# Performance work log

Measured on AMD Instinct MI355X. Metric: run time of the kernel, lower is better.

## Reference

```python
import jax, jax.numpy as jnp
import numpy as np

B, T, SD, DD = 256, 365, 64, 16
H, NH, L, FF = 256, 8, 4, 1024
K, P, N = 5, 30, 10000
DEG = np.pi / 180.0


def _ln(x, g, b):
    mu = x.mean(-1, keepdims=True)
    var = ((x - mu) ** 2).mean(-1, keepdims=True)
    return g * (x - mu) / jnp.sqrt(var + 1e-5) + b


def _gelu(x):
    return jax.nn.gelu(x, approximate=False)


def _forward(static, dynamic, lat, lon, all_statics, station_coords,
             W_st, b_st, g_st, be_st, W_dy, b_dy, g_dy, be_dy,
             Wqkv, bqkv, Wo, bo, g_ln1, be_ln1, Wf1, bf1, Wf2, bf2, g_ln2, be_ln2,
             W_o1, b_o1, W_o2, b_o2, scale, shift):
    # denormalize to CONUS degrees, then radians (as BallTree haversine expects)
    lat_o = (lat + 1.0) / 2.0 * (49.0 - 24.0) + 24.0
    lon_o = (lon + 1.0) / 2.0 * (-66.5 + 125.0) - 125.0
    qlat = lat_o[:, 0] * DEG
    qlon = lon_o[:, 0] * DEG
    slat = station_coords[:, 0]
    slon = station_coords[:, 1]
    dlat = qlat[:, None] - slat[None, :]
    dlon = qlon[:, None] - slon[None, :]
    # haversine term; true distance = 2*asin(sqrt(hav)) is monotone in hav,
    # so ranking by hav reproduces BallTree(metric='haversine') neighbor order
    hav = jnp.sin(dlat / 2) ** 2 + jnp.cos(qlat)[:, None] * jnp.cos(slat)[None, :] * jnp.sin(dlon / 2) ** 2
    _, nbr = jax.lax.top_k(-hav, K + 1)          # [B, K+1] nearest stations
    nbr = nbr[:, 1:]                              # drop self (nearest), keep K
    neigh = all_statics[nbr].reshape(static.shape[0], K * SD)  # gather + flatten
    combined = jnp.concatenate([static, neigh], axis=-1)       # [B, (K+1)*SD]

    sfeat = _gelu(_ln(combined @ W_st + b_st, g_st, be_st))    # static_net (dropout=eval)
    x = _gelu(_ln(dynamic @ W_dy + b_dy, g_dy, be_dy)) + sfeat[:, None, :]

    hd = H // NH
    inv_sqrt_d = 1.0 / jnp.sqrt(jnp.float32(hd))
    Bq, Tq = x.shape[0], x.shape[1]
    for l in range(L):  # post-norm TransformerEncoderLayer, relu FF
        qkv = x @ Wqkv[l] + bqkv[l]
        q, k, v = jnp.split(qkv, 3, axis=-1)
        q = q.reshape(Bq, Tq, NH, hd)
        k = k.reshape(Bq, Tq, NH, hd)
        v = v.reshape(Bq, Tq, NH, hd)
        att = jax.nn.softmax(jnp.einsum('bqhd,bkhd->bhqk', q, k) * inv_sqrt_d, axis=-1)
        ao = jnp.einsum('bhqk,bkhd->bqhd', att, v).reshape(Bq, Tq, H) @ Wo[l] + bo[l]
        x = _ln(x + ao, g_ln1[l], be_ln1[l])
        ff = jax.nn.relu(x @ Wf1[l] + bf1[l]) @ Wf2[l] + bf2[l]
        x = _ln(x + ff, g_ln2[l], be_ln2[l])

    pooled = x.mean(axis=1)
    raw = jnp.tanh(_gelu((pooled + sfeat) @ W_o1 + b_o1) @ W_o2 + b_o2)
    return raw * scale + shift


def setup_inputs() -> dict:
    key = jax.random.key(0)
    ks = jax.random.split(key, 24)
    rn = lambda k, shp: jax.random.normal(k, shp, jnp.float32) * 0.02
    inp = {}
    inp['static'] = jax.random.normal(ks[0], (B, SD), jnp.float32)
    inp['dynamic'] = jax.random.normal(ks[1], (B, T, DD), jnp.float32)
    inp['lat'] = jax.random.uniform(ks[2], (B, 1), jnp.float32, -1.0, 1.0)
    inp['lon'] = jax.random.uniform(ks[3], (B, 1), jnp.float32, -1.0, 1.0)
    inp['all_statics'] = jax.random.normal(ks[4], (N, SD), jnp.float32)
    slat = jax.random.uniform(ks[5], (N,), jnp.float32, 24.0, 49.0) * DEG
    slon = jax.random.uniform(ks[6], (N,), jnp.float32, -125.0, -66.5) * DEG
    inp['station_coords'] = jnp.stack([slat, slon], axis=-1)
    # static_net
    inp['W_st'] = rn(ks[7], (SD * (K + 1), H)); inp['b_st'] = jnp.zeros(H)
    inp['g_st'] = jnp.ones(H); inp['be_st'] = jnp.zeros(H)
    # dynamic_emb
    inp['W_dy'] = rn(ks[8], (DD, H)); inp['b_dy'] = jnp.zeros(H)
    inp['g_dy'] = jnp.ones(H); inp['be_dy'] = jnp.zeros(H)
    # transformer (stacked over layers)
    inp['Wqkv'] = rn(ks[9], (L, H, 3 * H)); inp['bqkv'] = jnp.zeros((L, 3 * H))
    inp['Wo'] = rn(ks[10], (L, H, H)); inp['bo'] = jnp.zeros((L, H))
    inp['g_ln1'] = jnp.ones((L, H)); inp['be_ln1'] = jnp.zeros((L, H))
    inp['Wf1'] = rn(ks[11], (L, H, FF)); inp['bf1'] = jnp.zeros((L, FF))
    inp['Wf2'] = rn(ks[12], (L, FF, H)); inp['bf2'] = jnp.zeros((L, H))
    inp['g_ln2'] = jnp.ones((L, H)); inp['be_ln2'] = jnp.zeros((L, H))
    # output head
    inp['W_o1'] = rn(ks[13], (H, H // 2)); inp['b_o1'] = jnp.zeros(H // 2)
    inp['W_o2'] = rn(ks[14], (H // 2, P)); inp['b_o2'] = jnp.zeros(P)
    inp['scale'] = jnp.array(1.0, jnp.float32)
    inp['shift'] = jnp.array(0.0, jnp.float32)
    return inp


def reference(static, dynamic, lat, lon, all_statics, station_coords,
              W_st, b_st, g_st, be_st, W_dy, b_dy, g_dy, be_dy,
              Wqkv, bqkv, Wo, bo, g_ln1, be_ln1, Wf1, bf1, Wf2, bf2, g_ln2, be_ln2,
              W_o1, b_o1, W_o2, b_o2, scale, shift):
    return _forward(static, dynamic, lat, lon, all_statics, station_coords,
                    W_st, b_st, g_st, be_st, W_dy, b_dy, g_dy, be_dy,
                    Wqkv, bqkv, Wo, bo, g_ln1, be_ln1, Wf1, bf1, Wf2, bf2, g_ln2, be_ln2,
                    W_o1, b_o1, W_o2, b_o2, scale, shift)
```

## Files before the change

kernel.cpp:

```cpp
#include <hip/hip_runtime.h>
#include <math.h>

#define T_SEQ 365
#define HDIM 256
#define NHEADS 8
#define HD 32
#define BATCH 256
#define DDIM 16
#define FFDIM 1024
#define NST 10000
#define KNB 5
#define SDIM 64

typedef __bf16 bf16x8 __attribute__((ext_vector_type(8)));
typedef float  f32x16 __attribute__((ext_vector_type(16)));
typedef unsigned short u16x8 __attribute__((ext_vector_type(8)));

__device__ __forceinline__ ushort f2b_hi(float v) {
    unsigned u = __float_as_uint(v);
    unsigned r = u + 0x7fffu + ((u >> 16) & 1u);
    return (ushort)(r >> 16);
}
__device__ __forceinline__ float b2f(ushort h) {
    return __uint_as_float(((unsigned)h) << 16);
}
__device__ __forceinline__ ushort f2b_lo(float v, ushort hi) {
    return f2b_hi(v - b2f(hi));
}

__device__ __forceinline__ float gelu_f(float x) {
    return 0.5f * x * (1.f + erff(x * 0.70710678118654752f));
}


__device__ __forceinline__ float block_sum256(float v, float* sred) {
    #pragma unroll
    for (int off = 32; off; off >>= 1) v += __shfl_xor(v, off);
    int wave = threadIdx.x >> 6;
    if ((threadIdx.x & 63) == 0) sred[wave] = v;
    __syncthreads();
    float s = sred[0] + sred[1] + sred[2] + sred[3];
    __syncthreads();
    return s;
}

__global__ __launch_bounds__(256) void topk_kernel(
    const float* __restrict__ lat, const float* __restrict__ lon,
    const float* __restrict__ coords, int* __restrict__ nbr)
{
    __shared__ float hav[NST];
    __shared__ float rv[256];
    __shared__ int   ri[256];
    const float DEG = 0.017453292519943295f;
    int b = blockIdx.x, t = threadIdx.x;
    float lat_o = (lat[b] + 1.f) * 0.5f * 25.f + 24.f;
    float lon_o = (lon[b] + 1.f) * 0.5f * 58.5f - 125.f;
    float qlat = lat_o * DEG, qlon = lon_o * DEG;
    float cq = cosf(qlat);
    for (int i = t; i < NST; i += 256) {
        float slat = coords[2*i], slon = coords[2*i+1];
        float dlat = qlat - slat, dlon = qlon - slon;
        float s1 = sinf(dlat * 0.5f), s2 = sinf(dlon * 0.5f);
        hav[i] = s1*s1 + cq * cosf(slat) * s2*s2;
    }
    __syncthreads();
    for (int sel = 0; sel < KNB + 1; ++sel) {
        float bv = 1e30f; int bi = 0x7fffffff;
        for (int i = t; i < NST; i += 256) {
            float v = hav[i];
            if (v < bv || (v == bv && i < bi)) { bv = v; bi = i; }
        }
        rv[t] = bv; ri[t] = bi;
        __syncthreads();
        for (int s = 128; s > 0; s >>= 1) {
            if (t < s) {
                float ov = rv[t+s]; int oi = ri[t+s];
                if (ov < rv[t] || (ov == rv[t] && oi < ri[t])) { rv[t] = ov; ri[t] = oi; }
            }
            __syncthreads();
        }
        if (t == 0) {
            if (sel > 0) nbr[b*KNB + sel - 1] = ri[0];
            hav[ri[0]] = 1e30f;
        }
        __syncthreads();
    }
}

__global__ __launch_bounds__(256) void sfeat_kernel(
    const float* __restrict__ stat, const float* __restrict__ all_st,
    const int* __restrict__ nbr, const float* __restrict__ W,
    const float* __restrict__ bias, const float* __restrict__ g,
    const float* __restrict__ be, float* __restrict__ sfeat)
{
    __shared__ float comb[(KNB+1)*SDIM];
    __shared__ float sred[4];
    int b = blockIdx.x, t = threadIdx.x;
    for (int i = t; i < (KNB+1)*SDIM; i += 256) {
        if (i < SDIM) comb[i] = stat[b*SDIM + i];
        else {
            int n = (i - SDIM) >> 6, d = (i - SDIM) & 63;
            comb[i] = all_st[(size_t)nbr[b*KNB + n] * SDIM + d];
        }
    }
    __syncthreads();
    float acc = bias[t];
    for (int j = 0; j < (KNB+1)*SDIM; ++j)
        acc = fmaf(comb[j], W[j*HDIM + t], acc);
    float mu  = block_sum256(acc, sred) * (1.f/256.f);
    float d   = acc - mu;
    float var = block_sum256(d*d, sred) * (1.f/256.f);
    float y = g[t] * d * rsqrtf(var + 1e-5f) + be[t];
    sfeat[(size_t)b*HDIM + t] = gelu_f(y);
}

__global__ __launch_bounds__(256) void dyn_kernel(
    const float* __restrict__ dynv, const float* __restrict__ W,
    const float* __restrict__ bias, const float* __restrict__ g,
    const float* __restrict__ be, const float* __restrict__ sfeat,
    ushort* __restrict__ xhi, ushort* __restrict__ xlo)
{
    __shared__ float w[DDIM*HDIM];
    __shared__ float dr[4][DDIM];
    int wave = threadIdx.x >> 6, lane = threadIdx.x & 63;
    int row0 = blockIdx.x * 4;
    for (int i = threadIdx.x; i < DDIM*HDIM; i += 256) w[i] = W[i];
    if (lane < DDIM)
        dr[wave][lane] = dynv[(size_t)(row0 + wave)*DDIM + lane];
    __syncthreads();
    int row = row0 + wave;
    int b = row / T_SEQ;
    int c0 = lane * 4;
    float v0 = bias[c0], v1 = bias[c0+1], v2 = bias[c0+2], v3 = bias[c0+3];
    #pragma unroll
    for (int k = 0; k < DDIM; ++k) {
        float dk = dr[wave][k];
        float4 wv = *reinterpret_cast<const float4*>(&w[k*HDIM + c0]);
        v0 = fmaf(dk, wv.x, v0); v1 = fmaf(dk, wv.y, v1);
        v2 = fmaf(dk, wv.z, v2); v3 = fmaf(dk, wv.w, v3);
    }
    float s = v0 + v1 + v2 + v3;
    #pragma unroll
    for (int off = 32; off; off >>= 1) s += __shfl_xor(s, off);
    float mu = s * (1.f/256.f);
    float d0 = v0-mu, d1 = v1-mu, d2 = v2-mu, d3 = v3-mu;
    float s2 = d0*d0 + d1*d1 + d2*d2 + d3*d3;
    #pragma unroll
    for (int off = 32; off; off >>= 1) s2 += __shfl_xor(s2, off);
    float rs = rsqrtf(s2 * (1.f/256.f) + 1e-5f);
    float4 gg = *reinterpret_cast<const float4*>(&g[c0]);
    float4 bb = *reinterpret_cast<const float4*>(&be[c0]);
    float4 sf = *reinterpret_cast<const float4*>(&sfeat[(size_t)b*HDIM + c0]);
    float o0 = gelu_f(gg.x*d0*rs + bb.x) + sf.x;
    float o1 = gelu_f(gg.y*d1*rs + bb.y) + sf.y;
    float o2 = gelu_f(gg.z*d2*rs + bb.z) + sf.z;
    float o3 = gelu_f(gg.w*d3*rs + bb.w) + sf.w;
    size_t o = ((size_t)(row >> 5) * 32 + (c0 >> 3)) * 256 + ((row & 31) << 3) + (c0 & 7);
    ushort4 hv, lv;
    hv.x = f2b_hi(o0); lv.x = f2b_lo(o0, hv.x);
    hv.y = f2b_hi(o1); lv.y = f2b_lo(o1, hv.y);
    hv.z = f2b_hi(o2); lv.z = f2b_lo(o2, hv.z);
    hv.w = f2b_hi(o3); lv.w = f2b_lo(o3, hv.w);
    *reinterpret_cast<ushort4*>(&xhi[o]) = hv;
    *reinterpret_cast<ushort4*>(&xlo[o]) = lv;
}

__global__ __launch_bounds__(256) void tsplit_kernel(
    const float* __restrict__ W, ushort* __restrict__ hi, ushort* __restrict__ lo,
    int K, int N)
{
    __shared__ float tile[32][33];
    size_t l = blockIdx.z;
    const float* Wl = W + l*(size_t)K*N;
    ushort* hil = hi + l*(size_t)K*N;
    ushort* lol = lo + l*(size_t)K*N;
    int n0 = blockIdx.x*32, k0 = blockIdx.y*32;
    int tx = threadIdx.x & 31, ty = threadIdx.x >> 5;
    int KB = K >> 3;
    for (int i = ty; i < 32; i += 8) tile[i][tx] = Wl[(size_t)(k0+i)*N + n0 + tx];
    __syncthreads();
    for (int i = ty; i < 32; i += 8) {
        float v = tile[tx][i];
        ushort h = f2b_hi(v);
        size_t o = ((size_t)(n0 >> 5) * KB + (k0 >> 3) + (tx >> 3)) * 256
                 + ((size_t)i << 3) + (tx & 7);
        hil[o] = h;
        lol[o] = f2b_lo(v, h);
    }
}

template<int DO_RELU, int OUT>
__global__ __launch_bounds__(256) void gemm_mfma(
    const ushort* __restrict__ Ahi, const ushort* __restrict__ Alo,
    const ushort* __restrict__ Bhi, const ushort* __restrict__ Blo,
    const float* __restrict__ bias,
    ushort* __restrict__ Chi, ushort* __restrict__ Clo,
    ushort* __restrict__ Wq_h, ushort* __restrict__ Wq_l,
    ushort* __restrict__ Wk_h, ushort* __restrict__ Wk_l,
    ushort* __restrict__ Wv_h, ushort* __restrict__ Wv_l,
    int M, int N, int K)
{
    const int t = threadIdx.x;
    const int lane = t & 63, wave = t >> 6;
    const int wr = wave >> 1, wc = wave & 1;
    const int lr = lane & 31, kg = lane >> 5;
    const int row_b = blockIdx.y * 128 + wr * 64;
    const int col_b = blockIdx.x * 128 + wc * 64;
    const int KB = K >> 3;

    const ushort *pAh[2], *pAl[2], *pBh[2], *pBl[2];
    #pragma unroll
    for (int mi = 0; mi < 2; ++mi) {
        int rb = row_b + mi*32; if (rb > M - 32) rb = M - 32;
        size_t base = ((size_t)(rb >> 5) * KB + kg) * 256 + lr * 8;
        pAh[mi] = Ahi + base; pAl[mi] = Alo + base;
    }
    #pragma unroll
    for (int nj = 0; nj < 2; ++nj) {
        size_t base = ((size_t)((col_b + nj*32) >> 5) * KB + kg) * 256 + lr * 8;
        pBh[nj] = Bhi + base; pBl[nj] = Blo + base;
    }

    f32x16 acc[2][2];
    #pragma unroll
    for (int i = 0; i < 2; ++i)
        #pragma unroll
        for (int j = 0; j < 2; ++j)
            #pragma unroll
            for (int r = 0; r < 16; ++r) acc[i][j][r] = 0.f;

    bf16x8 a0h[2], a0l[2], b0h[2], b0l[2];
    bf16x8 a1h[2], a1l[2], b1h[2], b1l[2];

#define LOADF(AH, AL, BH, BL, OFF) do {                                        \
    _Pragma("unroll") for (int mi = 0; mi < 2; ++mi) {                         \
        AH[mi] = *reinterpret_cast<const bf16x8*>(pAh[mi] + (OFF));            \
        AL[mi] = *reinterpret_cast<const bf16x8*>(pAl[mi] + (OFF)); }          \
    _Pragma("unroll") for (int nj = 0; nj < 2; ++nj) {                         \
        BH[nj] = *reinterpret_cast<const bf16x8*>(pBh[nj] + (OFF));            \
        BL[nj] = *reinterpret_cast<const bf16x8*>(pBl[nj] + (OFF)); } } while(0)

#define MFMAF(AH, AL, BH, BL) do {                                             \
    _Pragma("unroll") for (int mi = 0; mi < 2; ++mi)                           \
    _Pragma("unroll") for (int nj = 0; nj < 2; ++nj) {                         \
        acc[mi][nj] = __builtin_amdgcn_mfma_f32_32x32x16_bf16(                 \
            AH[mi], BH[nj], acc[mi][nj], 0, 0, 0);                             \
        acc[mi][nj] = __builtin_amdgcn_mfma_f32_32x32x16_bf16(                 \
            AH[mi], BL[nj], acc[mi][nj], 0, 0, 0);                             \
        acc[mi][nj] = __builtin_amdgcn_mfma_f32_32x32x16_bf16(                 \
            AL[mi], BH[nj], acc[mi][nj], 0, 0, 0); } } while(0)

    LOADF(a0h, a0l, b0h, b0l, 0);
    for (int k0 = 0; k0 < K; k0 += 32) {
        size_t o1 = (size_t)((k0 + 16) >> 3) * 256;
        LOADF(a1h, a1l, b1h, b1l, o1);
        MFMAF(a0h, a0l, b0h, b0l);
        size_t o2 = (k0 + 32 < K) ? (size_t)((k0 + 32) >> 3) * 256 : 0;
        LOADF(a0h, a0l, b0h, b0l, o2);
        MFMAF(a1h, a1l, b1h, b1l);
    }
#undef LOADF
#undef MFMAF

    #pragma unroll
    for (int mi = 0; mi < 2; ++mi) {
        int rb2 = row_b + mi*32;
        #pragma unroll
        for (int nj = 0; nj < 2; ++nj) {
            int colf = col_b + nj*32 + lr;
            float bv = bias[colf];
            if (OUT == 1) {
                size_t ftb = ((size_t)(rb2 >> 5) * (N >> 3) + (colf >> 3)) * 256 + (colf & 7);
                #pragma unroll
                for (int r = 0; r < 16; ++r) {
                    int r31 = (r & 3) + 8*(r >> 2) + 4*kg;
                    int row = rb2 + r31;
                    if (row >= M) continue;
                    float v = acc[mi][nj][r] + bv;
                    if (DO_RELU) v = fmaxf(v, 0.f);
                    size_t oo = ftb + (size_t)r31 * 8;
                    ushort hh = f2b_hi(v);
                    Chi[oo] = hh;
                    Clo[oo] = f2b_lo(v, hh);
                }
            } else {
                int sel = (col_b + nj*32) >> 8;
                int h = (colf >> 5) & 7;
                int d = colf & 31;
                #pragma unroll
                for (int r = 0; r < 16; ++r) {
                    int r31 = (r & 3) + 8*(r >> 2) + 4*kg;
                    int row = rb2 + r31;
                    if (row >= M) continue;
                    float v = acc[mi][nj][r] + bv;
                    int bl = row / T_SEQ;
                    int tok = row - bl * T_SEQ;
                    size_t bb = (size_t)(bl*8 + h) * 12288;
                    ushort hh = f2b_hi(v);
                    ushort ll = f2b_lo(v, hh);
                    if (sel == 0) {
                        size_t o = bb + (size_t)((tok >> 5)*4 + (d >> 3))*256
                                 + ((tok & 31) << 3) + (d & 7);
                        Wq_h[o] = hh; Wq_l[o] = ll;
                    } else if (sel == 1) {
                        size_t o = bb + (size_t)((tok >> 5)*4 + (d >> 3))*256
                                 + ((tok & 31) << 3) + (d & 7);
                        Wk_h[o] = hh; Wk_l[o] = ll;
                    } else {
                        size_t o = bb + (size_t)(tok >> 3)*256 + d*8 + (tok & 7);
                        Wv_h[o] = hh; Wv_l[o] = ll;
                    }
                }
            }
        }
    }
}

__global__ __launch_bounds__(256) void gemm_ln(
    const ushort* __restrict__ Ahi, const ushort* __restrict__ Alo,
    const ushort* __restrict__ Bhi, const ushort* __restrict__ Blo,
    const float* __restrict__ bias,
    ushort* __restrict__ xhi, ushort* __restrict__ xlo,
    const float* __restrict__ g, const float* __restrict__ be,
    int M, int K)
{
    const int N = HDIM;
    const int t = threadIdx.x;
    const int lane = t & 63, wave = t >> 6;
    const int lr = lane & 31, kg = lane >> 5;
    const int row_b = blockIdx.y * 32;
    const int col_w = wave * 64;
    const int KB = K >> 3;

    const ushort *pAh, *pAl, *pBh[2], *pBl[2];
    {
        size_t base = ((size_t)(row_b >> 5) * KB + kg) * 256 + lr * 8;
        pAh = Ahi + base; pAl = Alo + base;
    }
    #pragma unroll
    for (int nj = 0; nj < 2; ++nj) {
        size_t base = ((size_t)((col_w + nj*32) >> 5) * KB + kg) * 256 + lr * 8;
        pBh[nj] = Bhi + base; pBl[nj] = Blo + base;
    }

    f32x16 acc[2];
    #pragma unroll
    for (int j = 0; j < 2; ++j)
        #pragma unroll
        for (int r = 0; r < 16; ++r) acc[j][r] = 0.f;

    bf16x8 a0h, a0l, b0h[2], b0l[2];
    bf16x8 a1h, a1l, b1h[2], b1l[2];

#define LOADF(AH, AL, BH, BL, OFF) do {                                        \
    AH = *reinterpret_cast<const bf16x8*>(pAh + (OFF));                        \
    AL = *reinterpret_cast<const bf16x8*>(pAl + (OFF));                        \
    _Pragma("unroll") for (int nj = 0; nj < 2; ++nj) {                         \
        BH[nj] = *reinterpret_cast<const bf16x8*>(pBh[nj] + (OFF));            \
        BL[nj] = *reinterpret_cast<const bf16x8*>(pBl[nj] + (OFF)); } } while(0)

#define MFMAF(AH, AL, BH, BL) do {                                             \
    _Pragma("unroll") for (int nj = 0; nj < 2; ++nj) {                         \
        acc[nj] = __builtin_amdgcn_mfma_f32_32x32x16_bf16(                     \
            AH, BH[nj], acc[nj], 0, 0, 0);                                     \
        acc[nj] = __builtin_amdgcn_mfma_f32_32x32x16_bf16(                     \
            AH, BL[nj], acc[nj], 0, 0, 0);                                     \
        acc[nj] = __builtin_amdgcn_mfma_f32_32x32x16_bf16(                     \
            AL, BH[nj], acc[nj], 0, 0, 0); } } while(0)

    LOADF(a0h, a0l, b0h, b0l, 0);
    for (int k0 = 0; k0 < K; k0 += 32) {
        size_t o1 = (size_t)((k0 + 16) >> 3) * 256;
        LOADF(a1h, a1l, b1h, b1l, o1);
        MFMAF(a0h, a0l, b0h, b0l);
        size_t o2 = (k0 + 32 < K) ? (size_t)((k0 + 32) >> 3) * 256 : 0;
        LOADF(a0h, a0l, b0h, b0l, o2);
        MFMAF(a1h, a1l, b1h, b1l);
    }
#undef LOADF
#undef MFMAF

    float s1[16], s2[16];
    #pragma unroll
    for (int nj = 0; nj < 2; ++nj) {
        int col = col_w + nj*32 + lr;
        float bv = bias[col];
        #pragma unroll
        for (int r = 0; r < 16; ++r) {
            int r31 = (r & 3) + 8*(r >> 2) + 4*kg;
            int row = row_b + r31;
            size_t oo = ((size_t)(row >> 5) * (N >> 3) + (col >> 3)) * 256
                      + ((row & 31) << 3) + (col & 7);
            float v = acc[nj][r] + bv + b2f(xhi[oo]) + b2f(xlo[oo]);
            acc[nj][r] = v;
            if (nj == 0) { s1[r] = v;  s2[r] = v*v; }
            else         { s1[r] += v; s2[r] += v*v; }
        }
    }
    #pragma unroll
    for (int r = 0; r < 16; ++r) {
        #pragma unroll
        for (int off = 1; off <= 16; off <<= 1) {
            s1[r] += __shfl_xor(s1[r], off);
            s2[r] += __shfl_xor(s2[r], off);
        }
    }
    __shared__ float red1[4][32];
    __shared__ float red2[4][32];
    __shared__ float tot1[32];
    __shared__ float tot2[32];
    if (lr == 0) {
        #pragma unroll
        for (int r = 0; r < 16; ++r) {
            int rr = (r & 3) + 8*(r >> 2) + 4*kg;
            red1[wave][rr] = s1[r];
            red2[wave][rr] = s2[r];
        }
    }
    __syncthreads();
    if (t < 32) {
        tot1[t] = red1[0][t] + red1[1][t] + red1[2][t] + red1[3][t];
        tot2[t] = red2[0][t] + red2[1][t] + red2[2][t] + red2[3][t];
    }
    __syncthreads();
    #pragma unroll
    for (int r = 0; r < 16; ++r) {
        int r31 = (r & 3) + 8*(r >> 2) + 4*kg;
        int row = row_b + r31;
        float mu = tot1[r31] * (1.f/256.f);
        float var = fmaf(-mu, mu, tot2[r31] * (1.f/256.f));
        float rs = rsqrtf(var + 1e-5f);
        #pragma unroll
        for (int nj = 0; nj < 2; ++nj) {
            int col = col_w + nj*32 + lr;
            float o = g[col] * (acc[nj][r] - mu) * rs + be[col];
            size_t oo = ((size_t)(row >> 5) * (N >> 3) + (col >> 3)) * 256
                      + ((row & 31) << 3) + (col & 7);
            ushort hh = f2b_hi(o);
            xhi[oo] = hh;
            xlo[oo] = f2b_lo(o, hh);
        }
    }
}

__global__ __launch_bounds__(256) void attn_mfma(
    const ushort* __restrict__ Qh, const ushort* __restrict__ Ql,
    const ushort* __restrict__ Kh, const ushort* __restrict__ Kl,
    const ushort* __restrict__ Vh, const ushort* __restrict__ Vl,
    ushort* __restrict__ ahi, ushort* __restrict__ alo)
{
    const int bh = blockIdx.y;
    const int wave = threadIdx.x >> 6, lane = threadIdx.x & 63;
    const int qt = blockIdx.x * 4 + wave;
    const int lr = lane & 31, kg = lane >> 5;
    const size_t base = (size_t)bh * 12288;
    const float scale = 0.17677669529663687f;

    bf16x8 qfh[2], qfl[2];
    #pragma unroll
    for (int ks = 0; ks < 2; ++ks) {
        size_t o = base + (size_t)(qt*4 + ks*2 + kg)*256 + lr*8;
        qfh[ks] = *reinterpret_cast<const bf16x8*>(Qh + o);
        qfl[ks] = *reinterpret_cast<const bf16x8*>(Ql + o);
    }

    float m = -3e38f;
    for (int kt = 0; kt < 12; ++kt) {
        f32x16 st;
        #pragma unroll
        for (int r = 0; r < 16; ++r) st[r] = 0.f;
        #pragma unroll
        for (int ks = 0; ks < 2; ++ks) {
            size_t o = base + (size_t)(kt*4 + ks*2 + kg)*256 + lr*8;
            bf16x8 kfh = *reinterpret_cast<const bf16x8*>(Kh + o);
            bf16x8 kfl = *reinterpret_cast<const bf16x8*>(Kl + o);
            st = __builtin_amdgcn_mfma_f32_32x32x16_bf16(kfh, qfh[ks], st, 0,0,0);
            st = __builtin_amdgcn_mfma_f32_32x32x16_bf16(kfh, qfl[ks], st, 0,0,0);
            st = __builtin_amdgcn_mfma_f32_32x32x16_bf16(kfl, qfh[ks], st, 0,0,0);
        }
        #pragma unroll
        for (int r = 0; r < 16; ++r) {
            int krow = kt*32 + (r & 3) + 8*(r >> 2) + 4*kg;
            m = fmaxf(m, (krow < T_SEQ) ? st[r] : -3e38f);
        }
    }
    m = fmaxf(m, __shfl_xor(m, 32));

    f32x16 oacc;
    #pragma unroll
    for (int r = 0; r < 16; ++r) oacc[r] = 0.f;
    float l = 0.f;

    for (int kt = 0; kt < 12; ++kt) {
        f32x16 st;
        #pragma unroll
        for (int r = 0; r < 16; ++r) st[r] = 0.f;
        #pragma unroll
        for (int ks = 0; ks < 2; ++ks) {
            size_t o = base + (size_t)(kt*4 + ks*2 + kg)*256 + lr*8;
            bf16x8 kfh = *reinterpret_cast<const bf16x8*>(Kh + o);
            bf16x8 kfl = *reinterpret_cast<const bf16x8*>(Kl + o);
            st = __builtin_amdgcn_mfma_f32_32x32x16_bf16(kfh, qfh[ks], st, 0,0,0);
            st = __builtin_amdgcn_mfma_f32_32x32x16_bf16(kfh, qfl[ks], st, 0,0,0);
            st = __builtin_amdgcn_mfma_f32_32x32x16_bf16(kfl, qfh[ks], st, 0,0,0);
        }
        float p[16];
        #pragma unroll
        for (int r = 0; r < 16; ++r) {
            int krow = kt*32 + (r & 3) + 8*(r >> 2) + 4*kg;
            float sv = (krow < T_SEQ) ? st[r] : -3e38f;
            float e = __expf((sv - m) * scale);
            p[r] = e; l += e;
        }
        float pp[16];
        #pragma unroll
        for (int r = 0; r < 16; ++r) pp[r] = __shfl_xor(p[r], 32);
        #pragma unroll
        for (int ks = 0; ks < 2; ++ks) {
            union { u16x8 u; bf16x8 b; } fh, fl;
            #pragma unroll
            for (int j = 0; j < 8; ++j) {
                float e;
                if (ks == 0)
                    e = kg ? ((j < 4) ? pp[4+j] : p[j])
                           : ((j < 4) ? p[j]    : pp[j-4]);
                else
                    e = kg ? ((j < 4) ? pp[12+j] : p[8+j])
                           : ((j < 4) ? p[8+j]   : pp[4+j]);
                ushort hh = f2b_hi(e);
                fh.u[j] = hh;
                fl.u[j] = f2b_lo(e, hh);
            }
            size_t vo = base + (size_t)(kt*4 + ks*2 + kg)*256 + lr*8;
            bf16x8 vfh = *reinterpret_cast<const bf16x8*>(Vh + vo);
            bf16x8 vfl = *reinterpret_cast<const bf16x8*>(Vl + vo);
            oacc = __builtin_amdgcn_mfma_f32_32x32x16_bf16(fh.b, vfh, oacc, 0,0,0);
            oacc = __builtin_amdgcn_mfma_f32_32x32x16_bf16(fh.b, vfl, oacc, 0,0,0);
            oacc = __builtin_amdgcn_mfma_f32_32x32x16_bf16(fl.b, vfh, oacc, 0,0,0);
        }
    }
    l += __shfl_xor(l, 32);
    float il = 1.f / l;

    const int bl = bh >> 3, h = bh & 7;
    #pragma unroll
    for (int r = 0; r < 16; ++r) {
        int q = (r & 3) + 8*(r >> 2) + 4*kg;
        float sc = __shfl(il, q);
        int row_local = qt*32 + q;
        if (row_local < T_SEQ) {
            float v = oacc[r] * sc;
            int grow = bl*T_SEQ + row_local;
            int col = h*32 + lr;
            size_t o = ((size_t)(grow >> 5)*32 + (col >> 3))*256
                     + ((grow & 31) << 3) + (col & 7);
            ushort hh = f2b_hi(v);
            ahi[o] = hh;
            alo[o] = f2b_lo(v, hh);
        }
    }
}

__global__ __launch_bounds__(256) void head_kernel(
    const ushort* __restrict__ xhi, const ushort* __restrict__ xlo,
    const float* __restrict__ sfeat,
    const float* __restrict__ W1, const float* __restrict__ b1,
    const float* __restrict__ W2, const float* __restrict__ b2,
    const float* __restrict__ scale, const float* __restrict__ shift,
    float* __restrict__ out)
{
    __shared__ float p[HDIM];
    __shared__ float h1[HDIM/2];
    int b = blockIdx.x, t = threadIdx.x;
    float acc = 0.f;
    for (int tt = 0; tt < T_SEQ; ++tt) {
        size_t row = (size_t)b*T_SEQ + tt;
        size_t o = ((row >> 5) * 32 + (t >> 3)) * 256 + ((row & 31) << 3) + (t & 7);
        acc += b2f(xhi[o]) + b2f(xlo[o]);
    }
    p[t] = acc * (1.f/365.f) + sfeat[(size_t)b*HDIM + t];
    __syncthreads();
    if (t < HDIM/2) {
        float a = b1[t];
        for (int c = 0; c < HDIM; ++c) a = fmaf(p[c], W1[c*(HDIM/2) + t], a);
        h1[t] = gelu_f(a);
    }
    __syncthreads();
    if (t < 30) {
        float a = b2[t];
        for (int j = 0; j < HDIM/2; ++j) a = fmaf(h1[j], W2[j*30 + t], a);
        out[b*30 + t] = tanhf(a) * scale[0] + shift[0];
    }
}

extern "C" void kernel_launch(void* const* d_in, const int* in_sizes, int n_in,
                              void* d_out, int out_size, void* d_ws, size_t ws_size,
                              hipStream_t stream) {
    const float* p_static = (const float*)d_in[0];
    const float* p_dyn    = (const float*)d_in[1];
    const float* p_lat    = (const float*)d_in[2];
    const float* p_lon    = (const float*)d_in[3];
    const float* p_all    = (const float*)d_in[4];
    const float* p_coords = (const float*)d_in[5];
    const float* p_Wst    = (const float*)d_in[6];
    const float* p_bst    = (const float*)d_in[7];
    const float* p_gst    = (const float*)d_in[8];
    const float* p_best   = (const float*)d_in[9];
    const float* p_Wdy    = (const float*)d_in[10];
    const float* p_bdy    = (const float*)d_in[11];
    const float* p_gdy    = (const float*)d_in[12];
    const float* p_bedy   = (const float*)d_in[13];
    const float* p_Wqkv   = (const float*)d_in[14];
    const float* p_bqkv   = (const float*)d_in[15];
    const float* p_Wo     = (const float*)d_in[16];
    const float* p_bo     = (const float*)d_in[17];
    const float* p_gln1   = (const float*)d_in[18];
    const float* p_beln1  = (const float*)d_in[19];
    const float* p_Wf1    = (const float*)d_in[20];
    const float* p_bf1    = (const float*)d_in[21];
    const float* p_Wf2    = (const float*)d_in[22];
    const float* p_bf2    = (const float*)d_in[23];
    const float* p_gln2   = (const float*)d_in[24];
    const float* p_beln2  = (const float*)d_in[25];
    const float* p_Wo1    = (const float*)d_in[26];
    const float* p_bo1    = (const float*)d_in[27];
    const float* p_Wo2    = (const float*)d_in[28];
    const float* p_bo2    = (const float*)d_in[29];
    const float* p_scale  = (const float*)d_in[30];
    const float* p_shift  = (const float*)d_in[31];
    float* out = (float*)d_out;
    (void)in_sizes; (void)n_in; (void)out_size;

    char* ws = (char*)d_ws;
    size_t off = 0;
    auto alloc = [&](size_t bytes) -> void* {
        void* p = ws + off;
        off += (bytes + 255) & ~(size_t)255;
        return p;
    };
    const int ROWS = BATCH * T_SEQ;
    int*    nbr   = (int*)   alloc((size_t)BATCH*KNB*sizeof(int));
    float*  sfeat = (float*) alloc((size_t)BATCH*HDIM*sizeof(float));
    ushort* xhi   = (ushort*)alloc((size_t)ROWS*HDIM*sizeof(ushort));
    ushort* xlo   = (ushort*)alloc((size_t)ROWS*HDIM*sizeof(ushort));
    const size_t SZ_QKV = (size_t)4*768*256, SZ_O = (size_t)4*256*256;
    const size_t SZ_F1  = (size_t)4*1024*256, SZ_F2 = (size_t)4*256*1024;
    ushort* Wqkvt_h = (ushort*)alloc(SZ_QKV*2*sizeof(ushort)); ushort* Wqkvt_l = Wqkvt_h + SZ_QKV;
    ushort* Wot_h   = (ushort*)alloc(SZ_O  *2*sizeof(ushort)); ushort* Wot_l   = Wot_h   + SZ_O;
    ushort* Wf1t_h  = (ushort*)alloc(SZ_F1 *2*sizeof(ushort)); ushort* Wf1t_l  = Wf1t_h  + SZ_F1;
    ushort* Wf2t_h  = (ushort*)alloc(SZ_F2 *2*sizeof(ushort)); ushort* Wf2t_l  = Wf2t_h  + SZ_F2;
    size_t fixed = off;

    const size_t PER_B = (size_t)T_SEQ * 1024 * 4;
    const size_t PER_A = (size_t)T_SEQ * 256 * 4;
    const size_t PER_CH = PER_B + PER_A;
    int CH = 32;
    {
        const int tiers[5] = {256, 192, 128, 96, 64};
        for (int i = 0; i < 5; ++i) {
            if (fixed + (size_t)tiers[i]*PER_CH + 8192 <= ws_size) { CH = tiers[i]; break; }
        }
    }
    char*   big    = (char*)alloc((size_t)CH * PER_B);
    ushort* aatt_h = (ushort*)alloc((size_t)CH * PER_A);
    const int RW = CH * T_SEQ;
    ushort* aatt_l = aatt_h + (size_t)RW * HDIM;
    const size_t seg = (size_t)CH * 8 * 12288;
    ushort* Qh  = (ushort*)big;
    ushort* Ql  = Qh  + seg;
    ushort* Kh2 = Ql  + seg;
    ushort* Kl2 = Kh2 + seg;
    ushort* Vth = Kl2 + seg;
    ushort* Vtl = Vth + seg;
    ushort* hbuf_h = (ushort*)big;
    ushort* hbuf_l = hbuf_h + (size_t)RW * FFDIM;
    const int GY  = (RW + 127) / 128;
    const int GY3 = RW / 32;

    topk_kernel <<<BATCH, 256, 0, stream>>>(p_lat, p_lon, p_coords, nbr);
    sfeat_kernel<<<BATCH, 256, 0, stream>>>(p_static, p_all, nbr, p_Wst, p_bst, p_gst, p_best, sfeat);
    dyn_kernel  <<<ROWS/4, 256, 0, stream>>>(p_dyn, p_Wdy, p_bdy, p_gdy, p_bedy, sfeat, xhi, xlo);
    tsplit_kernel<<<dim3(24, 8, 4), 256, 0, stream>>>(p_Wqkv, Wqkvt_h, Wqkvt_l, 256, 768);
    tsplit_kernel<<<dim3( 8, 8, 4), 256, 0, stream>>>(p_Wo,   Wot_h,   Wot_l,   256, 256);
    tsplit_kernel<<<dim3(32, 8, 4), 256, 0, stream>>>(p_Wf1,  Wf1t_h,  Wf1t_l,  256, 1024);
    tsplit_kernel<<<dim3( 8,32, 4), 256, 0, stream>>>(p_Wf2,  Wf2t_h,  Wf2t_l,  1024, 256);

    const int NCHUNK = BATCH / CH;
    for (int c = 0; c < NCHUNK; ++c) {
        size_t co = (size_t)c * CH * T_SEQ * HDIM;
        ushort* xhic = xhi + co;
        ushort* xloc = xlo + co;
        for (int l = 0; l < 4; ++l) {
            gemm_mfma<0,2><<<dim3(6, GY), 256, 0, stream>>>(
                xhic, xloc, Wqkvt_h + (size_t)l*768*256, Wqkvt_l + (size_t)l*768*256,
                p_bqkv + l*768, nullptr, nullptr,
                Qh, Ql, Kh2, Kl2, Vth, Vtl, RW, 768, 256);
            attn_mfma<<<dim3(3, CH*8), 256, 0, stream>>>(
                Qh, Ql, Kh2, Kl2, Vth, Vtl, aatt_h, aatt_l);
            gemm_ln<<<dim3(1, GY3), 256, 0, stream>>>(
                aatt_h, aatt_l, Wot_h + (size_t)l*256*256, Wot_l + (size_t)l*256*256,
                p_bo + l*256, xhic, xloc, p_gln1 + l*256, p_beln1 + l*256, RW, 256);
            gemm_mfma<1,1><<<dim3(8, GY), 256, 0, stream>>>(
                xhic, xloc, Wf1t_h + (size_t)l*1024*256, Wf1t_l + (size_t)l*1024*256,
                p_bf1 + l*1024, hbuf_h, hbuf_l,
                nullptr, nullptr, nullptr, nullptr, nullptr, nullptr, RW, 1024, 256);
            gemm_ln<<<dim3(1, GY3), 256, 0, stream>>>(
                hbuf_h, hbuf_l, Wf2t_h + (size_t)l*256*1024, Wf2t_l + (size_t)l*256*1024,
                p_bf2 + l*256, xhic, xloc, p_gln2 + l*256, p_beln2 + l*256, RW, 1024);
        }
    }
    head_kernel<<<BATCH, 256, 0, stream>>>(xhi, xlo, sfeat, p_Wo1, p_bo1, p_Wo2, p_bo2, p_scale, p_shift, out);
}
```

Baseline: 4.988 ms.

## Use single-pass online softmax in attention and chunk the activation buffer

The attention kernel now computes scores once per key tile with a running max and rescaling, replacing a separate pass that recomputed QK^T just to find the max. The residual stream buffer is allocated per chunk, with the embedding and mean-pooling moved inside the chunk loop. The attention output buffer now shares the scratch region, which may let larger chunks fit. The trade-off is extra per-tile rescale shuffles and exp calls.

```diff
diff --git a/kernel.cpp b/kernel.cpp
--- a/kernel.cpp
+++ b/kernel.cpp
@@ -117,7 +117,7 @@
 __global__ __launch_bounds__(256) void dyn_kernel(
     const float* __restrict__ dynv, const float* __restrict__ W,
     const float* __restrict__ bias, const float* __restrict__ g,
-    const float* __restrict__ be, const float* __restrict__ sfeat,
+    const float* __restrict__ be, const float* __restrict__ sfeatc,
     ushort* __restrict__ xhi, ushort* __restrict__ xlo)
 {
     __shared__ float w[DDIM*HDIM];
@@ -150,7 +150,7 @@
     float rs = rsqrtf(s2 * (1.f/256.f) + 1e-5f);
     float4 gg = *reinterpret_cast<const float4*>(&g[c0]);
     float4 bb = *reinterpret_cast<const float4*>(&be[c0]);
-    float4 sf = *reinterpret_cast<const float4*>(&sfeat[(size_t)b*HDIM + c0]);
+    float4 sf = *reinterpret_cast<const float4*>(&sfeatc[(size_t)b*HDIM + c0]);
     float o0 = gelu_f(gg.x*d0*rs + bb.x) + sf.x;
     float o1 = gelu_f(gg.y*d1*rs + bb.y) + sf.y;
     float o2 = gelu_f(gg.z*d2*rs + bb.z) + sf.z;
@@ -464,7 +464,11 @@
         qfl[ks] = *reinterpret_cast<const bf16x8*>(Ql + o);
     }
 
-    float m = -3e38f;
+    float m = -3e38f, l = 0.f;
+    f32x16 oacc;
+    #pragma unroll
+    for (int r = 0; r < 16; ++r) oacc[r] = 0.f;
+
     for (int kt = 0; kt < 12; ++kt) {
         f32x16 st;
         #pragma unroll
@@ -478,39 +482,31 @@
             st = __builtin_amdgcn_mfma_f32_32x32x16_bf16(kfh, qfl[ks], st, 0,0,0);
             st = __builtin_amdgcn_mfma_f32_32x32x16_bf16(kfl, qfh[ks], st, 0,0,0);
         }
+        float p[16];
+        float tm = -3e38f;
         #pragma unroll
         for (int r = 0; r < 16; ++r) {
             int krow = kt*32 + (r & 3) + 8*(r >> 2) + 4*kg;
-            m = fmaxf(m, (krow < T_SEQ) ? st[r] : -3e38f);
-        }
-    }
-    m = fmaxf(m, __shfl_xor(m, 32));
-
-    f32x16 oacc;
-    #pragma unroll
-    for (int r = 0; r < 16; ++r) oacc[r] = 0.f;
-    float l = 0.f;
-
-    for (int kt = 0; kt < 12; ++kt) {
-        f32x16 st;
-        #pragma unroll
-        for (int r = 0; r < 16; ++r) st[r] = 0.f;
-        #pragma unroll
-        for (int ks = 0; ks < 2; ++ks) {
-            size_t o = base + (size_t)(kt*4 + ks*2 + kg)*256 + lr*8;
-            bf16x8 kfh = *reinterpret_cast<const bf16x8*>(Kh + o);
-            bf16x8 kfl = *reinterpret_cast<const bf16x8*>(Kl + o);
-            st = __builtin_amdgcn_mfma_f32_32x32x16_bf16(kfh, qfh[ks], st, 0,0,0);
-            st = __builtin_amdgcn_mfma_f32_32x32x16_bf16(kfh, qfl[ks], st, 0,0,0);
-            st = __builtin_amdgcn_mfma_f32_32x32x16_bf16(kfl, qfh[ks], st, 0,0,0);
-        }
-        float p[16];
+            p[r] = (krow < T_SEQ) ? st[r] : -3e38f;
+            tm = fmaxf(tm, p[r]);
+        }
+        tm = fmaxf(tm, __shfl_xor(tm, 32));
+        float newm = fmaxf(m, tm);
+        float f = __expf((m - newm) * scale);
+        m = newm;
+        l *= f;
+        float sumL = 0.f;
         #pragma unroll
         for (int r = 0; r < 16; ++r) {
-            int krow = kt*32 + (r & 3) + 8*(r >> 2) + 4*kg;
-            float sv = (krow < T_SEQ) ? st[r] : -3e38f;
-            float e = __expf((sv - m) * scale);
-            p[r] = e; l += e;
+            float e = __expf((p[r] - m) * scale);
+            p[r] = e; sumL += e;
+        }
+        l += sumL;
+        #pragma unroll
+        for (int r = 0; r < 16; ++r) {
+            int r31 = (r & 3) + 8*(r >> 2) + 4*kg;
+            float fr = __shfl(f, r31);
+            oacc[r] *= fr;
         }
         float pp[16];
         #pragma unroll
@@ -561,16 +557,10 @@
     }
 }
 
-__global__ __launch_bounds__(256) void head_kernel(
+__global__ __launch_bounds__(256) void pool_kernel(
     const ushort* __restrict__ xhi, const ushort* __restrict__ xlo,
-    const float* __restrict__ sfeat,
-    const float* __restrict__ W1, const float* __restrict__ b1,
-    const float* __restrict__ W2, const float* __restrict__ b2,
-    const float* __restrict__ scale, const float* __restrict__ shift,
-    float* __restrict__ out)
-{
-    __shared__ float p[HDIM];
-    __shared__ float h1[HDIM/2];
+    float* __restrict__ pooled)
+{
     int b = blockIdx.x, t = threadIdx.x;
     float acc = 0.f;
     for (int tt = 0; tt < T_SEQ; ++tt) {
@@ -578,7 +568,20 @@
         size_t o = ((row >> 5) * 32 + (t >> 3)) * 256 + ((row & 31) << 3) + (t & 7);
         acc += b2f(xhi[o]) + b2f(xlo[o]);
     }
-    p[t] = acc * (1.f/365.f) + sfeat[(size_t)b*HDIM + t];
+    pooled[(size_t)b*HDIM + t] = acc * (1.f/365.f);
+}
+
+__global__ __launch_bounds__(256) void head_kernel(
+    const float* __restrict__ pooled, const float* __restrict__ sfeat,
+    const float* __restrict__ W1, const float* __restrict__ b1,
+    const float* __restrict__ W2, const float* __restrict__ b2,
+    const float* __restrict__ scale, const float* __restrict__ shift,
+    float* __restrict__ out)
+{
+    __shared__ float p[HDIM];
+    __shared__ float h1[HDIM/2];
+    int b = blockIdx.x, t = threadIdx.x;
+    p[t] = pooled[(size_t)b*HDIM + t] + sfeat[(size_t)b*HDIM + t];
     __syncthreads();
     if (t < HDIM/2) {
         float a = b1[t];
@@ -638,11 +641,9 @@
         off += (bytes + 255) & ~(size_t)255;
         return p;
     };
-    const int ROWS = BATCH * T_SEQ;
-    int*    nbr   = (int*)   alloc((size_t)BATCH*KNB*sizeof(int));
-    float*  sfeat = (float*) alloc((size_t)BATCH*HDIM*sizeof(float));
-    ushort* xhi   = (ushort*)alloc((size_t)ROWS*HDIM*sizeof(ushort));
-    ushort* xlo   = (ushort*)alloc((size_t)ROWS*HDIM*sizeof(ushort));
+    int*    nbr    = (int*)   alloc((size_t)BATCH*KNB*sizeof(int));
+    float*  sfeat  = (float*) alloc((size_t)BATCH*HDIM*sizeof(float));
+    float*  pooled = (float*) alloc((size_t)BATCH*HDIM*sizeof(float));
     const size_t SZ_QKV = (size_t)4*768*256, SZ_O = (size_t)4*256*256;
     const size_t SZ_F1  = (size_t)4*1024*256, SZ_F2 = (size_t)4*256*1024;
     ushort* Wqkvt_h = (ushort*)alloc(SZ_QKV*2*sizeof(ushort)); ushort* Wqkvt_l = Wqkvt_h + SZ_QKV;
@@ -651,20 +652,20 @@
     ushort* Wf2t_h  = (ushort*)alloc(SZ_F2 *2*sizeof(ushort)); ushort* Wf2t_l  = Wf2t_h  + SZ_F2;
     size_t fixed = off;
 
-    const size_t PER_B = (size_t)T_SEQ * 1024 * 4;
-    const size_t PER_A = (size_t)T_SEQ * 256 * 4;
-    const size_t PER_CH = PER_B + PER_A;
+    const size_t X_CH   = (size_t)T_SEQ * HDIM * 4;
+    const size_t REG_CH = (size_t)1553408;
+    const size_t PER_CH = X_CH + REG_CH;
     int CH = 32;
     {
-        const int tiers[5] = {256, 192, 128, 96, 64};
-        for (int i = 0; i < 5; ++i) {
+        const int tiers[3] = {256, 128, 64};
+        for (int i = 0; i < 3; ++i) {
             if (fixed + (size_t)tiers[i]*PER_CH + 8192 <= ws_size) { CH = tiers[i]; break; }
         }
     }
-    char*   big    = (char*)alloc((size_t)CH * PER_B);
-    ushort* aatt_h = (ushort*)alloc((size_t)CH * PER_A);
     const int RW = CH * T_SEQ;
-    ushort* aatt_l = aatt_h + (size_t)RW * HDIM;
+    ushort* xh  = (ushort*)alloc((size_t)CH * X_CH);
+    ushort* xl  = xh + (size_t)RW * HDIM;
+    char*   big = (char*)alloc((size_t)CH * REG_CH);
     const size_t seg = (size_t)CH * 8 * 12288;
     ushort* Qh  = (ushort*)big;
     ushort* Ql  = Qh  + seg;
@@ -672,6 +673,8 @@
     ushort* Kl2 = Kh2 + seg;
     ushort* Vth = Kl2 + seg;
     ushort* Vtl = Vth + seg;
+    ushort* aatt_h = Vtl + seg;
+    ushort* aatt_l = aatt_h + (size_t)RW * HDIM;
     ushort* hbuf_h = (ushort*)big;
     ushort* hbuf_l = hbuf_h + (size_t)RW * FFDIM;
     const int GY  = (RW + 127) / 128;
@@ -679,7 +682,6 @@
 
     topk_kernel <<<BATCH, 256, 0, stream>>>(p_lat, p_lon, p_coords, nbr);
     sfeat_kernel<<<BATCH, 256, 0, stream>>>(p_static, p_all, nbr, p_Wst, p_bst, p_gst, p_best, sfeat);
-    dyn_kernel  <<<ROWS/4, 256, 0, stream>>>(p_dyn, p_Wdy, p_bdy, p_gdy, p_bedy, sfeat, xhi, xlo);
     tsplit_kernel<<<dim3(24, 8, 4), 256, 0, stream>>>(p_Wqkv, Wqkvt_h, Wqkvt_l, 256, 768);
     tsplit_kernel<<<dim3( 8, 8, 4), 256, 0, stream>>>(p_Wo,   Wot_h,   Wot_l,   256, 256);
     tsplit_kernel<<<dim3(32, 8, 4), 256, 0, stream>>>(p_Wf1,  Wf1t_h,  Wf1t_l,  256, 1024);
@@ -687,27 +689,28 @@
 
     const int NCHUNK = BATCH / CH;
     for (int c = 0; c < NCHUNK; ++c) {
-        size_t co = (size_t)c * CH * T_SEQ * HDIM;
-        ushort* xhic = xhi + co;
-        ushort* xloc = xlo + co;
+        dyn_kernel<<<RW/4, 256, 0, stream>>>(
+            p_dyn + (size_t)c*CH*T_SEQ*DDIM, p_Wdy, p_bdy, p_gdy, p_bedy,
+            sfeat + (size_t)c*CH*HDIM, xh, xl);
         for (int l = 0; l < 4; ++l) {
             gemm_mfma<0,2><<<dim3(6, GY), 256, 0, stream>>>(
-                xhic, xloc, Wqkvt_h + (size_t)l*768*256, Wqkvt_l + (size_t)l*768*256,
+                xh, xl, Wqkvt_h + (size_t)l*768*256, Wqkvt_l + (size_t)l*768*256,
                 p_bqkv + l*768, nullptr, nullptr,
                 Qh, Ql, Kh2, Kl2, Vth, Vtl, RW, 768, 256);
             attn_mfma<<<dim3(3, CH*8), 256, 0, stream>>>(
                 Qh, Ql, Kh2, Kl2, Vth, Vtl, aatt_h, aatt_l);
             gemm_ln<<<dim3(1, GY3), 256, 0, stream>>>(
                 aatt_h, aatt_l, Wot_h + (size_t)l*256*256, Wot_l + (size_t)l*256*256,
-                p_bo + l*256, xhic, xloc, p_gln1 + l*256, p_beln1 + l*256, RW, 256);
+                p_bo + l*256, xh, xl, p_gln1 + l*256, p_beln1 + l*256, RW, 256);
             gemm_mfma<1,1><<<dim3(8, GY), 256, 0, stream>>>(
-                xhic, xloc, Wf1t_h + (size_t)l*1024*256, Wf1t_l + (size_t)l*1024*256,
+                xh, xl, Wf1t_h + (size_t)l*1024*256, Wf1t_l + (size_t)l*1024*256,
                 p_bf1 + l*1024, hbuf_h, hbuf_l,
                 nullptr, nullptr, nullptr, nullptr, nullptr, nullptr, RW, 1024, 256);
             gemm_ln<<<dim3(1, GY3), 256, 0, stream>>>(
                 hbuf_h, hbuf_l, Wf2t_h + (size_t)l*256*1024, Wf2t_l + (size_t)l*256*1024,
-                p_bf2 + l*256, xhic, xloc, p_gln2 + l*256, p_beln2 + l*256, RW, 1024);
-        }
-    }
-    head_kernel<<<BATCH, 256, 0, stream>>>(xhi, xlo, sfeat, p_Wo1, p_bo1, p_Wo2, p_bo2, p_scale, p_shift, out);
-}
+                p_bf2 + l*256, xh, xl, p_gln2 + l*256, p_beln2 + l*256, RW, 1024);
+        }
+        pool_kernel<<<CH, 256, 0, stream>>>(xh, xl, pooled + (size_t)c*CH*HDIM);
+    }
+    head_kernel<<<BATCH, 256, 0, stream>>>(pooled, sfeat, p_Wo1, p_bo1, p_Wo2, p_bo2, p_scale, p_shift, out);
+}
```

After: 4.584 ms. -8.1%, faster.
